# Kernel optimization log

Measured on AMD Instinct MI355X. Metric: run time of the kernel, lower is better.

## Reference

```python
import jax, jax.numpy as jnp
import numpy as np

NQ, NL, PD, B = 4, 2, 64, 524288
RANGES = [1, 2]  # StronglyEntanglingLayers default: (l % (nq-1)) + 1


def setup_inputs() -> dict:
    key = jax.random.key(0)
    ks = jax.random.split(key, 4)
    x = jax.random.normal(ks[0], (B, NQ), jnp.float32)
    # PennyLane TorchLayer default init: uniform [0, 2pi)
    weights = jax.random.uniform(ks[1], (NL, NQ, 3), jnp.float32, 0.0, 2.0 * np.pi)
    W = jax.random.normal(ks[2], (PD, NQ), jnp.float32) / np.sqrt(NQ)
    b = jnp.zeros((PD,), jnp.float32)
    gamma = jnp.ones((PD,), jnp.float32)
    beta = jnp.zeros((PD,), jnp.float32)
    return {"x": x, "weights": weights, "W": W, "b": b, "gamma": gamma, "beta": beta}


def _apply_1q_batched(state, gate, w):
    # state: [B, 2,2,2,2], gate: [B,2,2], act on wire w (axis w+1)
    s = jnp.moveaxis(state, w + 1, -1)
    s = jnp.einsum('bij,b...j->b...i', gate, s)
    return jnp.moveaxis(s, -1, w + 1)


def _apply_1q_shared(state, gate, w):
    s = jnp.moveaxis(state, w + 1, -1)
    s = jnp.einsum('ij,b...j->b...i', gate, s)
    return jnp.moveaxis(s, -1, w + 1)


def _cnot(state, c, t):
    s = jnp.moveaxis(state, (c + 1, t + 1), (-2, -1))
    s = jnp.stack([s[..., 0, :], s[..., 1, ::-1]], axis=-2)  # flip target where control=1
    return jnp.moveaxis(s, (-2, -1), (c + 1, t + 1))


def _rot(phi, theta, omega):
    # Rot = RZ(omega) RY(theta) RZ(phi)
    ct, st = jnp.cos(theta / 2), jnp.sin(theta / 2)
    ep = jnp.exp(-0.5j * (phi + omega))
    em = jnp.exp(-0.5j * (phi - omega))
    return jnp.array([[ep * ct, -jnp.conj(em) * st],
                      [em * st, jnp.conj(ep) * ct]])


def _circuit(x, weights):
    n = x.shape[0]
    state = jnp.zeros((n,) + (2,) * NQ, jnp.complex64)
    state = state.at[(slice(None),) + (0,) * NQ].set(1.0)
    # AngleEmbedding (RX rotations)
    half = x * 0.5
    c, s = jnp.cos(half), jnp.sin(half)
    for w in range(NQ):
        cw, sw = c[:, w], -1j * s[:, w]
        g = jnp.stack([jnp.stack([cw + 0j, sw], -1),
                       jnp.stack([sw, cw + 0j], -1)], -2)  # [B,2,2]
        state = _apply_1q_batched(state, g, w)
    # StronglyEntanglingLayers
    for l in range(NL):
        for w in range(NQ):
            state = _apply_1q_shared(state, _rot(weights[l, w, 0], weights[l, w, 1], weights[l, w, 2]), w)
        r = RANGES[l]
        for w in range(NQ):
            state = _cnot(state, w, (w + r) % NQ)
    probs = state.real ** 2 + state.imag ** 2  # [B,2,2,2,2]
    zs = []
    for w in range(NQ):
        other = tuple(a for a in range(1, NQ + 1) if a != w + 1)
        m = probs.sum(other)  # [B,2]
        zs.append(m[:, 0] - m[:, 1])  # <Z_w>
    return jnp.stack(zs, -1)  # [B,4]


def reference(x, weights, W, b, gamma, beta):
    xt = jnp.tanh(x) * jnp.pi
    q = _circuit(xt, weights)
    q = jax.nn.softmax(q, axis=-1)
    h = q @ W.T + b  # [B, 64]
    mu = h.mean(-1, keepdims=True)
    var = ((h - mu) ** 2).mean(-1, keepdims=True)
    return (h - mu) / jnp.sqrt(var + 1e-5) * gamma + beta
```

## Files before the change

kernel.cpp:

```cpp
#include <hip/hip_runtime.h>

#define BLK 256
#define PD 64
#define PI_F 3.14159265358979323846f

__device__ __forceinline__ float fast_tanh(float v) {
    float e = __expf(2.0f * v);
    return 1.0f - 2.0f / (e + 1.0f);
}

template<int M>
__device__ __forceinline__ void gate_apply(float* ar, float* ai,
        float u00r, float u00i, float u01r, float u01i,
        float u10r, float u10i, float u11r, float u11i) {
    #pragma unroll
    for (int i = 0; i < 16; ++i) {
        if (i & M) continue;
        const int j = i | M;
        const float a0r = ar[i], a0i = ai[i], a1r = ar[j], a1i = ai[j];
        ar[i] = u00r*a0r - u00i*a0i + u01r*a1r - u01i*a1i;
        ai[i] = u00r*a0i + u00i*a0r + u01r*a1i + u01i*a1r;
        ar[j] = u10r*a0r - u10i*a0i + u11r*a1r - u11i*a1i;
        ai[j] = u10r*a0i + u10i*a0r + u11r*a1i + u11i*a1r;
    }
}

template<int CM, int TM>
__device__ __forceinline__ void cnotg(float* ar, float* ai) {
    #pragma unroll
    for (int i = 0; i < 16; ++i) {
        if ((i & CM) && !(i & TM)) {
            const int j = i | TM;
            float tp;
            tp = ar[i]; ar[i] = ar[j]; ar[j] = tp;
            tp = ai[i]; ai[i] = ai[j]; ai[j] = tp;
        }
    }
}

extern "C" __global__ void __launch_bounds__(64)
qbranch_prep(const float* __restrict__ wts, const float* __restrict__ W,
             const float* __restrict__ bias, float* __restrict__ ws)
{
    const int t = threadIdx.x;
    const float4 wr = reinterpret_cast<const float4*>(W)[t];
    const float bp = bias[t];
    float v[20] = { wr.x*wr.x, wr.x*wr.y, wr.x*wr.z, wr.x*wr.w,
                    wr.y*wr.y, wr.y*wr.z, wr.y*wr.w,
                    wr.z*wr.z, wr.z*wr.w,
                    wr.w*wr.w,
                    wr.x*bp, wr.y*bp, wr.z*bp, wr.w*bp,
                    wr.x, wr.y, wr.z, wr.w,
                    bp, bp*bp };
    #pragma unroll
    for (int o = 32; o > 0; o >>= 1) {
        #pragma unroll
        for (int k = 0; k < 20; ++k) v[k] += __shfl_xor(v[k], o, 64);
    }
    if (t == 0) {
        #pragma unroll
        for (int k = 0; k < 20; ++k) ws[64 + k] = v[k] * (1.0f / 64.0f);
    }
    if (t < 8) {
        const float phi = wts[t * 3 + 0];
        const float th  = wts[t * 3 + 1];
        const float om  = wts[t * 3 + 2];
        float st, ct;  __sincosf(0.5f * th, &st, &ct);
        float sa, ca;  __sincosf(0.5f * (phi + om), &sa, &ca);
        float sb, cb;  __sincosf(0.5f * (phi - om), &sb, &cb);
        float* gg = ws + t * 8;
        gg[0] =  ct * ca;  gg[1] = -ct * sa;
        gg[2] = -st * cb;  gg[3] = -st * sb;
        gg[4] =  st * cb;  gg[5] = -st * sb;
        gg[6] =  ct * ca;  gg[7] =  ct * sa;
    }
}

extern "C" __global__ void __launch_bounds__(BLK)
qbranch_main(const float* __restrict__ x,
             const float* __restrict__ W,
             const float* __restrict__ bias,
             const float* __restrict__ gamma,
             const float* __restrict__ beta,
             const float* __restrict__ cw,
             float* __restrict__ out)
{
    __shared__ float4 sq4[BLK];
    __shared__ float2 sms[BLK];

    const int t = threadIdx.x;
    const int b = blockIdx.x * BLK + t;
    const float4 xv = reinterpret_cast<const float4*>(x)[b];

    float v0r[4], v0i[4], v1r[4], v1i[4];
    const float xs[4] = {xv.x, xv.y, xv.z, xv.w};
    #pragma unroll
    for (int w = 0; w < 4; ++w) {
        float s, c;
        __sincosf(0.5f * PI_F * fast_tanh(xs[w]), &s, &c);
        const float g0 = cw[w*8+0], g1 = cw[w*8+1], g2 = cw[w*8+2], g3 = cw[w*8+3];
        const float g4 = cw[w*8+4], g5 = cw[w*8+5], g6 = cw[w*8+6], g7 = cw[w*8+7];
        v0r[w] = fmaf(c, g0,  s * g3);
        v0i[w] = fmaf(c, g1, -s * g2);
        v1r[w] = fmaf(c, g4,  s * g7);
        v1i[w] = fmaf(c, g5, -s * g6);
    }

    float Ar[4], Ai[4], Br[4], Bi[4];
    #pragma unroll
    for (int j = 0; j < 4; ++j) {
        const int b0 = j >> 1, b1 = j & 1;
        const float p0r = b0 ? v1r[0] : v0r[0], p0i = b0 ? v1i[0] : v0i[0];
        const float p1r = b1 ? v1r[1] : v0r[1], p1i = b1 ? v1i[1] : v0i[1];
        Ar[j] = p0r*p1r - p0i*p1i;
        Ai[j] = p0r*p1i + p0i*p1r;
        const float p2r = b0 ? v1r[2] : v0r[2], p2i = b0 ? v1i[2] : v0i[2];
        const float p3r = b1 ? v1r[3] : v0r[3], p3i = b1 ? v1i[3] : v0i[3];
        Br[j] = p2r*p3r - p2i*p3i;
        Bi[j] = p2r*p3i + p2i*p3r;
    }
    float ar[16], ai[16];
    #pragma unroll
    for (int i = 0; i < 16; ++i) {
        const int hi = i >> 2, lo = i & 3;
        ar[i] = Ar[hi]*Br[lo] - Ai[hi]*Bi[lo];
        ai[i] = Ar[hi]*Bi[lo] + Ai[hi]*Br[lo];
    }

    cnotg<8, 4>(ar, ai);
    cnotg<4, 2>(ar, ai);
    cnotg<2, 1>(ar, ai);
    cnotg<1, 8>(ar, ai);

    gate_apply<8>(ar, ai, cw[32], cw[33], cw[34], cw[35], cw[36], cw[37], cw[38], cw[39]);
    gate_apply<4>(ar, ai, cw[40], cw[41], cw[42], cw[43], cw[44], cw[45], cw[46], cw[47]);
    gate_apply<2>(ar, ai, cw[48], cw[49], cw[50], cw[51], cw[52], cw[53], cw[54], cw[55]);
    gate_apply<1>(ar, ai, cw[56], cw[57], cw[58], cw[59], cw[60], cw[61], cw[62], cw[63]);

    cnotg<8, 2>(ar, ai);
    cnotg<4, 1>(ar, ai);
    cnotg<2, 8>(ar, ai);
    cnotg<1, 4>(ar, ai);

    float z0 = 0.f, z1 = 0.f, z2 = 0.f, z3 = 0.f;
    #pragma unroll
    for (int i = 0; i < 16; ++i) {
        const float p = ar[i]*ar[i] + ai[i]*ai[i];
        z0 += (i & 8) ? -p : p;
        z1 += (i & 4) ? -p : p;
        z2 += (i & 2) ? -p : p;
        z3 += (i & 1) ? -p : p;
    }
    const float mx = fmaxf(fmaxf(z0, z1), fmaxf(z2, z3));
    const float e0 = __expf(z0 - mx), e1 = __expf(z1 - mx);
    const float e2 = __expf(z2 - mx), e3 = __expf(z3 - mx);
    const float inv = 1.0f / (e0 + e1 + e2 + e3);
    const float q0 = e0 * inv, q1 = e1 * inv, q2 = e2 * inv, q3 = e3 * inv;

    const float* sS = cw + 64;
    const float mu = fmaf(q0, sS[14], fmaf(q1, sS[15], fmaf(q2, sS[16], fmaf(q3, sS[17], sS[18]))));
    const float t0 = sS[0]*q0 + sS[1]*q1 + sS[2]*q2 + sS[3]*q3 + 2.0f*sS[10];
    const float t1 = sS[1]*q0 + sS[4]*q1 + sS[5]*q2 + sS[6]*q3 + 2.0f*sS[11];
    const float t2 = sS[2]*q0 + sS[5]*q1 + sS[7]*q2 + sS[8]*q3 + 2.0f*sS[12];
    const float t3 = sS[3]*q0 + sS[6]*q1 + sS[8]*q2 + sS[9]*q3 + 2.0f*sS[13];
    const float Eh2 = t0*q0 + t1*q1 + t2*q2 + t3*q3 + sS[19];
    const float rstd = rsqrtf(Eh2 - mu * mu + 1e-5f);

    sq4[t] = make_float4(q0, q1, q2, q3);
    sms[t] = make_float2(mu, rstd);

    const int p4 = t & 15;
    const float4 w0 = reinterpret_cast<const float4*>(W)[p4 * 4 + 0];
    const float4 w1 = reinterpret_cast<const float4*>(W)[p4 * 4 + 1];
    const float4 w2 = reinterpret_cast<const float4*>(W)[p4 * 4 + 2];
    const float4 w3 = reinterpret_cast<const float4*>(W)[p4 * 4 + 3];
    const float4 bg = reinterpret_cast<const float4*>(bias)[p4];
    const float4 gm = reinterpret_cast<const float4*>(gamma)[p4];
    const float4 bt = reinterpret_cast<const float4*>(beta)[p4];

    __syncthreads();

    const int sub = t >> 4;
    const size_t base = (size_t)blockIdx.x * (BLK * PD);
    #pragma unroll 4
    for (int it = 0; it < 16; ++it) {
        const int row = it * 16 + sub;
        const float4 qv = sq4[row];
        const float2 ms = sms[row];
        const float h0 = fmaf(qv.x, w0.x, fmaf(qv.y, w0.y, fmaf(qv.z, w0.z, fmaf(qv.w, w0.w, bg.x))));
        const float h1 = fmaf(qv.x, w1.x, fmaf(qv.y, w1.y, fmaf(qv.z, w1.z, fmaf(qv.w, w1.w, bg.y))));
        const float h2 = fmaf(qv.x, w2.x, fmaf(qv.y, w2.y, fmaf(qv.z, w2.z, fmaf(qv.w, w2.w, bg.z))));
        const float h3 = fmaf(qv.x, w3.x, fmaf(qv.y, w3.y, fmaf(qv.z, w3.z, fmaf(qv.w, w3.w, bg.w))));
        float4 pk;
        pk.x = fmaf((h0 - ms.x), ms.y * gm.x, bt.x);
        pk.y = fmaf((h1 - ms.x), ms.y * gm.y, bt.y);
        pk.z = fmaf((h2 - ms.x), ms.y * gm.z, bt.z);
        pk.w = fmaf((h3 - ms.x), ms.y * gm.w, bt.w);
        *reinterpret_cast<float4*>(&out[base + (size_t)row * PD + p4 * 4]) = pk;
    }
}

extern "C" void kernel_launch(void* const* d_in, const int* in_sizes, int n_in,
                              void* d_out, int out_size, void* d_ws, size_t ws_size,
                              hipStream_t stream) {
    const float* x     = (const float*)d_in[0];
    const float* wts   = (const float*)d_in[1];
    const float* W     = (const float*)d_in[2];
    const float* bias  = (const float*)d_in[3];
    const float* gamma = (const float*)d_in[4];
    const float* beta  = (const float*)d_in[5];
    float* ws  = (float*)d_ws;
    float* out = (float*)d_out;
    const int B = in_sizes[0] / 4;
    hipLaunchKernelGGL(qbranch_prep, dim3(1), dim3(64), 0, stream, wts, W, bias, ws);
    hipLaunchKernelGGL(qbranch_main, dim3(B / BLK), dim3(BLK), 0, stream,
                       x, W, bias, gamma, beta, ws, out);
}
```

Baseline: 175.4 us.

## Split fused circuit kernel into separate circuit and epilogue kernels

Splits the single fused kernel in two. The first kernel computes the circuit, softmax and LayerNorm statistics and writes them to a workspace. The second kernel reads those values back and does the 64-wide projection, normalization and output store. The aim is to separate the register-heavy compute phase from the store-heavy epilogue so each can run at its own occupancy. The cost is an extra launch and a global round trip of about 24 bytes per row.

```diff
diff --git a/kernel.cpp b/kernel.cpp
--- a/kernel.cpp
+++ b/kernel.cpp
@@ -77,19 +77,12 @@
 }
 
 extern "C" __global__ void __launch_bounds__(BLK)
-qbranch_main(const float* __restrict__ x,
-             const float* __restrict__ W,
-             const float* __restrict__ bias,
-             const float* __restrict__ gamma,
-             const float* __restrict__ beta,
-             const float* __restrict__ cw,
-             float* __restrict__ out)
+qbranch_circuit(const float* __restrict__ x,
+                const float* __restrict__ cw,
+                float4* __restrict__ wq,
+                float2* __restrict__ wms)
 {
-    __shared__ float4 sq4[BLK];
-    __shared__ float2 sms[BLK];
-
-    const int t = threadIdx.x;
-    const int b = blockIdx.x * BLK + t;
+    const int b = blockIdx.x * BLK + threadIdx.x;
     const float4 xv = reinterpret_cast<const float4*>(x)[b];
 
     float v0r[4], v0i[4], v1r[4], v1i[4];
@@ -166,10 +159,24 @@
     const float Eh2 = t0*q0 + t1*q1 + t2*q2 + t3*q3 + sS[19];
     const float rstd = rsqrtf(Eh2 - mu * mu + 1e-5f);
 
-    sq4[t] = make_float4(q0, q1, q2, q3);
-    sms[t] = make_float2(mu, rstd);
-
+    wq[b]  = make_float4(q0, q1, q2, q3);
+    wms[b] = make_float2(mu, rstd);
+}
+
+extern "C" __global__ void __launch_bounds__(BLK)
+qbranch_epilogue(const float4* __restrict__ wq,
+                 const float2* __restrict__ wms,
+                 const float* __restrict__ W,
+                 const float* __restrict__ bias,
+                 const float* __restrict__ gamma,
+                 const float* __restrict__ beta,
+                 float* __restrict__ out)
+{
+    const int t = threadIdx.x;
     const int p4 = t & 15;
+    const int sub = t >> 4;
+    const int row0 = blockIdx.x * BLK;
+
     const float4 w0 = reinterpret_cast<const float4*>(W)[p4 * 4 + 0];
     const float4 w1 = reinterpret_cast<const float4*>(W)[p4 * 4 + 1];
     const float4 w2 = reinterpret_cast<const float4*>(W)[p4 * 4 + 2];
@@ -178,15 +185,12 @@
     const float4 gm = reinterpret_cast<const float4*>(gamma)[p4];
     const float4 bt = reinterpret_cast<const float4*>(beta)[p4];
 
-    __syncthreads();
-
-    const int sub = t >> 4;
-    const size_t base = (size_t)blockIdx.x * (BLK * PD);
+    const size_t base = (size_t)row0 * PD;
     #pragma unroll 4
     for (int it = 0; it < 16; ++it) {
-        const int row = it * 16 + sub;
-        const float4 qv = sq4[row];
-        const float2 ms = sms[row];
+        const int row = row0 + it * 16 + sub;
+        const float4 qv = wq[row];
+        const float2 ms = wms[row];
         const float h0 = fmaf(qv.x, w0.x, fmaf(qv.y, w0.y, fmaf(qv.z, w0.z, fmaf(qv.w, w0.w, bg.x))));
         const float h1 = fmaf(qv.x, w1.x, fmaf(qv.y, w1.y, fmaf(qv.z, w1.z, fmaf(qv.w, w1.w, bg.y))));
         const float h2 = fmaf(qv.x, w2.x, fmaf(qv.y, w2.y, fmaf(qv.z, w2.z, fmaf(qv.w, w2.w, bg.z))));
@@ -196,7 +200,7 @@
         pk.y = fmaf((h1 - ms.x), ms.y * gm.y, bt.y);
         pk.z = fmaf((h2 - ms.x), ms.y * gm.z, bt.z);
         pk.w = fmaf((h3 - ms.x), ms.y * gm.w, bt.w);
-        *reinterpret_cast<float4*>(&out[base + (size_t)row * PD + p4 * 4]) = pk;
+        *reinterpret_cast<float4*>(&out[base + (size_t)(it * 16 + sub) * PD + p4 * 4]) = pk;
     }
 }
 
@@ -212,7 +216,13 @@
     float* ws  = (float*)d_ws;
     float* out = (float*)d_out;
     const int B = in_sizes[0] / 4;
+
+    float4* wq  = (float4*)(ws + 256);
+    float2* wms = (float2*)(ws + 256 + 4 * (size_t)B);
+
     hipLaunchKernelGGL(qbranch_prep, dim3(1), dim3(64), 0, stream, wts, W, bias, ws);
-    hipLaunchKernelGGL(qbranch_main, dim3(B / BLK), dim3(BLK), 0, stream,
-                       x, W, bias, gamma, beta, ws, out);
-}
+    hipLaunchKernelGGL(qbranch_circuit, dim3(B / BLK), dim3(BLK), 0, stream,
+                       x, ws, wq, wms);
+    hipLaunchKernelGGL(qbranch_epilogue, dim3(B / BLK), dim3(BLK), 0, stream,
+                       wq, wms, W, bias, gamma, beta, out);
+}
```

Result: slower. 186.8 us (+6.5%).
